# Kernel optimization log

Hardware: AMD Instinct MI355X
Metric: run time of the kernel (lower is better)

## Reference

```python
import jax, jax.numpy as jnp
import numpy as np

NUM_LAYERS = 3
INPUT_SIZE = 64
EMB = 128
NUM_CAT = 128          # must equal EMB for the W_e_proj assignment to shape-check
NUM_QUERIES = 1
INIT_SCALE = 0.02
KERNEL_PARAM = 1.0     # referenced-but-undefined in source; standard alpha=1
B = 16
N = 2048
D = INPUT_SIZE + 2 * EMB                 # 320, transformer embedding dim
F_IN = INPUT_SIZE + NUM_CAT + EMB        # 320, raw input feature dim


def setup_inputs() -> dict:
    key = jax.random.key(0)
    k = jax.random.split(key, 6)
    x = jax.random.normal(k[0], (B, F_IN, N), dtype=jnp.float32)
    embedding_matrix = jax.random.normal(k[1], (EMB, NUM_CAT), dtype=jnp.float32)
    W_Q = jax.random.normal(k[2], (NUM_LAYERS, 1, D, D), dtype=jnp.float32) * INIT_SCALE
    W_K = jax.random.normal(k[3], (NUM_LAYERS, 1, D, D), dtype=jnp.float32) * INIT_SCALE
    W_V = jax.random.normal(k[4], (NUM_LAYERS, 1, D, D), dtype=jnp.float32) * INIT_SCALE
    P = jax.random.normal(k[5], (NUM_LAYERS, 1, D, D), dtype=jnp.float32) * INIT_SCALE
    return {"x": x, "embedding_matrix": embedding_matrix,
            "W_Q": W_Q, "W_K": W_K, "W_V": W_V, "P": P}


def _build_We(embedding_matrix):
    W = jnp.zeros((D, F_IN), dtype=embedding_matrix.dtype)
    W = W.at[:INPUT_SIZE, :INPUT_SIZE].set(jnp.eye(INPUT_SIZE, dtype=W.dtype))
    W = W.at[D - EMB:, F_IN - EMB:].set(jnp.eye(EMB, dtype=W.dtype))
    # rows [input_size : D-emb], cols [input_size : F-num_categories]
    W = W.at[INPUT_SIZE:D - EMB, INPUT_SIZE:F_IN - NUM_CAT].set(embedding_matrix)
    return W


def reference(x, embedding_matrix, W_Q, W_K, W_V, P):
    W = _build_We(embedding_matrix)
    h = jnp.einsum('df,bfn->bdn', W, x)                        # [B, D, N]
    for nl in range(NUM_LAYERS):
        key = h[:, :, :-NUM_QUERIES]                           # include_query=False
        value = key
        query = h
        n_context = key.shape[-1]
        Q = jnp.einsum('id,bdm->bim', W_Q[nl, 0], query)       # [B, D, N]
        K = jnp.einsum('id,bdn->bin', W_K[nl, 0], key)         # [B, D, M]
        V = jnp.einsum('id,bdn->bin', W_V[nl, 0], value)       # [B, D, M]
        # linear kernel scores
        scores = KERNEL_PARAM * jnp.einsum('bim,bin->bmn', Q, K)  # [B, N, M]
        attn = jnp.einsum('bin,bmn->bim', V, scores) / n_context  # [B, D, N]
        h = h + jnp.einsum('ji,bim->bjm', P[nl, 0], attn)
    f = h[:, -EMB:, :]                                         # [B, EMB, N] (squeeze no-op for B>1)
    logits = jnp.einsum('bdn,dc->bnc', f, embedding_matrix)    # [B, N, C]
    predictions = jax.nn.softmax(logits, axis=-1)
    return logits, predictions
```

## Files before the change

kernel.cpp:

```cpp
#include <hip/hip_runtime.h>
#include <math.h>

typedef long long ll;
typedef unsigned int uint;
typedef unsigned short ushort;
typedef __attribute__((ext_vector_type(4))) float f32x4;
typedef __attribute__((ext_vector_type(8))) short bf16x8;

#define SZ 102400LL
#define RS 40960LL

__device__ inline void split2(float v, ushort& h, ushort& l)
{
    uint u = __float_as_uint(v);
    uint uh = u + (0x7FFFu + ((u >> 16) & 1u));
    h = (ushort)(uh >> 16);
    float hf = __uint_as_float((uint)h << 16);
    float d = v - hf;
    uint ud = __float_as_uint(d);
    l = (ushort)((ud + (0x7FFFu + ((ud >> 16) & 1u))) >> 16);
}
__device__ inline float us2f(ushort h, ushort l)
{
    return __uint_as_float((uint)h << 16) + __uint_as_float((uint)l << 16);
}

__global__ __launch_bounds__(256) void gram_sp_k(
    const float* __restrict__ x, float* __restrict__ part,
    const float* __restrict__ Wq, const float* __restrict__ Wk,
    const float* __restrict__ Wv, const float* __restrict__ P,
    const float* __restrict__ emb,
    ushort* __restrict__ WqTs, ushort* __restrict__ WkTs, ushort* __restrict__ WvTs,
    ushort* __restrict__ Ps, ushort* __restrict__ embs, ushort* __restrict__ embTs,
    float* __restrict__ q0, ushort* __restrict__ xTh)
{
    __shared__ __align__(16) char smem[20480];
    int bid0 = blockIdx.x, tid = threadIdx.x;
    if (bid0 < 960) {
        ushort* Ah  = (ushort*)smem;
        ushort* Al_ = Ah + 2560;
        ushort* Bh  = Al_ + 2560;
        ushort* Bl_ = Bh + 2560;
        int flat = bid0;
        int swz = (flat & 7) * 120 + (flat >> 3);
        int b = swz / 60;
        int rr = swz - b * 60;
        int p = rr / 15, t = rr - p * 15;
        int ti = 0, rem = t;
        while (rem >= 5 - ti) { rem -= 5 - ti; ++ti; }
        int tj = ti + rem;
        int i0 = ti * 64, j0 = tj * 64;
        bool diag = (ti == tj);
        const float* X = x + (ll)b * 320 * 2048;
        int wv = tid >> 6, lane = tid & 63;
        int lr = lane & 15, kb = (lane >> 4) * 8;
        int cr = tid >> 2, ck = (tid & 3) * 8;
        f32x4 hh[4], hl[4], lh[4];
        f32x4 zz = {0.f, 0.f, 0.f, 0.f};
        #pragma unroll
        for (int f = 0; f < 4; ++f) { hh[f] = zz; hl[f] = zz; lh[f] = zz; }
        const ushort* BhS = diag ? Ah : Bh;
        const ushort* BlS = diag ? Al_ : Bl_;

        for (int it = 0; it < 16; ++it) {
            int kg0 = p * 512 + it * 32;
            {
                const float* src = X + (ll)(i0 + cr) * 2048 + kg0 + ck;
                float4 v0 = *(const float4*)src;
                float4 v1 = *(const float4*)(src + 4);
                float vals[8] = {v0.x,v0.y,v0.z,v0.w,v1.x,v1.y,v1.z,v1.w};
                if (kg0 + ck + 7 >= 2047) {
                    #pragma unroll
                    for (int u = 0; u < 8; ++u) if (kg0 + ck + u >= 2047) vals[u] = 0.f;
                }
                bf16x8 hv, lv;
                #pragma unroll
                for (int u = 0; u < 8; ++u) { ushort h, l; split2(vals[u], h, l);
                                              hv[u] = (short)h; lv[u] = (short)l; }
                *(bf16x8*)&Ah[cr * 40 + ck] = hv;
                *(bf16x8*)&Al_[cr * 40 + ck] = lv;
            }
            if (!diag) {
                const float* src = X + (ll)(j0 + cr) * 2048 + kg0 + ck;
                float4 v0 = *(const float4*)src;
                float4 v1 = *(const float4*)(src + 4);
                float vals[8] = {v0.x,v0.y,v0.z,v0.w,v1.x,v1.y,v1.z,v1.w};
                if (kg0 + ck + 7 >= 2047) {
                    #pragma unroll
                    for (int u = 0; u < 8; ++u) if (kg0 + ck + u >= 2047) vals[u] = 0.f;
                }
                bf16x8 hv, lv;
                #pragma unroll
                for (int u = 0; u < 8; ++u) { ushort h, l; split2(vals[u], h, l);
                                              hv[u] = (short)h; lv[u] = (short)l; }
                *(bf16x8*)&Bh[cr * 40 + ck] = hv;
                *(bf16x8*)&Bl_[cr * 40 + ck] = lv;
            }
            __syncthreads();
            if (xTh && diag) {
                int nl = tid >> 3, fq = (tid & 7) * 8;
                int n = kg0 + nl;
                bf16x8 v;
                #pragma unroll
                for (int u = 0; u < 8; ++u) v[u] = (short)Ah[(fq + u) * 40 + nl];
                if (n == 2047) {
                    #pragma unroll
                    for (int u = 0; u < 8; ++u) {
                        ushort h, l;
                        split2(X[(ll)(i0 + fq + u) * 2048 + 2047], h, l);
                        v[u] = (short)h;
                    }
                }
                *(bf16x8*)&xTh[((ll)b * 2048 + n) * 320 + i0 + fq] = v;
            }
            bf16x8 ah = *(const bf16x8*)&Ah[(wv * 16 + lr) * 40 + kb];
            bf16x8 al = *(const bf16x8*)&Al_[(wv * 16 + lr) * 40 + kb];
            #pragma unroll
            for (int f = 0; f < 4; ++f) {
                bf16x8 bh_ = *(const bf16x8*)&BhS[(f * 16 + lr) * 40 + kb];
                bf16x8 bl_ = *(const bf16x8*)&BlS[(f * 16 + lr) * 40 + kb];
                hh[f] = __builtin_amdgcn_mfma_f32_16x16x32_bf16(ah, bh_, hh[f], 0, 0, 0);
                hl[f] = __builtin_amdgcn_mfma_f32_16x16x32_bf16(ah, bl_, hl[f], 0, 0, 0);
                lh[f] = __builtin_amdgcn_mfma_f32_16x16x32_bf16(al, bh_, lh[f], 0, 0, 0);
            }
            __syncthreads();
        }
        float* out = part + (((ll)p * 16 + b) * 15 + t) * 4096;
        int orow0 = wv * 16 + (lane >> 4) * 4;
        #pragma unroll
        for (int f = 0; f < 4; ++f) {
            int col = f * 16 + lr;
            #pragma unroll
            for (int r = 0; r < 4; ++r)
                out[(orow0 + r) * 64 + col] = hh[f][r] + hl[f][r] + lh[f][r];
        }
        return;
    }
    int bid = bid0 - 960;
    float (*T)[65] = (float(*)[65])smem;
    if (bid < 225) {
        int m = bid / 25, t = bid % 25;
        const float* mats[3] = {Wq, Wk, Wv};
        ushort* dsts[3] = {WqTs, WkTs, WvTs};
        const float* src = mats[m / 3] + (ll)(m % 3) * SZ;
        ushort* dst = dsts[m / 3] + (ll)(m % 3) * SZ;
        int r0 = (t / 5) * 64, c0 = (t % 5) * 64;
        #pragma unroll
        for (int s = 0; s < 4; ++s) {
            int idx = s * 256 + tid;
            int r = idx >> 4, cq = (idx & 15) * 4;
            *(float4*)&T[r][cq] = *(const float4*)(src + (ll)(r0 + r) * 320 + c0 + cq);
        }
        __syncthreads();
        {
            int c = tid >> 2, kq = (tid & 3) * 16;
            bf16x8 h0, h1, l0, l1;
            #pragma unroll
            for (int u = 0; u < 8; ++u) {
                ushort h, l;
                split2(T[kq + u][c], h, l);     h0[u] = (short)h; l0[u] = (short)l;
                split2(T[kq + 8 + u][c], h, l); h1[u] = (short)h; l1[u] = (short)l;
            }
            ushort* dh = dst + (ll)(c0 + c) * 320 + r0 + kq;
            *(bf16x8*)dh = h0; *(bf16x8*)(dh + 8) = h1;
            *(bf16x8*)(dh + 3 * SZ) = l0; *(bf16x8*)(dh + 3 * SZ + 8) = l1;
        }
    } else if (bid < 375) {
        ll off = (ll)(bid - 225) * 2048 + tid * 8;
        float4 v0 = *(const float4*)(P + off);
        float4 v1 = *(const float4*)(P + off + 4);
        float vals[8] = {v0.x,v0.y,v0.z,v0.w,v1.x,v1.y,v1.z,v1.w};
        bf16x8 hv, lv;
        #pragma unroll
        for (int u = 0; u < 8; ++u) { ushort h,l; split2(vals[u],h,l);
                                      hv[u]=(short)h; lv[u]=(short)l; }
        *(bf16x8*)(Ps + off) = hv;
        *(bf16x8*)(Ps + off + 3 * SZ) = lv;
    } else if (bid < 383) {
        ll off = (ll)(bid - 375) * 2048 + tid * 8;
        float4 v0 = *(const float4*)(emb + off);
        float4 v1 = *(const float4*)(emb + off + 4);
        float vals[8] = {v0.x,v0.y,v0.z,v0.w,v1.x,v1.y,v1.z,v1.w};
        bf16x8 hv, lv;
        #pragma unroll
        for (int u = 0; u < 8; ++u) { ushort h,l; split2(vals[u],h,l);
                                      hv[u]=(short)h; lv[u]=(short)l; }
        *(bf16x8*)(embs + off) = hv;
        *(bf16x8*)(embs + off + 16384) = lv;
    } else if (bid < 387) {
        int t = bid - 383;
        int r0 = (t >> 1) * 64, c0 = (t & 1) * 64;
        {
            int r = tid >> 2, cq = (tid & 3) * 4;
            *(float4*)&T[r][cq]      = *(const float4*)(emb + (ll)(r0 + r) * 128 + c0 + cq);
            *(float4*)&T[r][cq + 16] = *(const float4*)(emb + (ll)(r0 + r) * 128 + c0 + cq + 16);
            *(float4*)&T[r][cq + 32] = *(const float4*)(emb + (ll)(r0 + r) * 128 + c0 + cq + 32);
            *(float4*)&T[r][cq + 48] = *(const float4*)(emb + (ll)(r0 + r) * 128 + c0 + cq + 48);
        }
        __syncthreads();
        {
            int c = tid >> 2, kq = (tid & 3) * 16;
            bf16x8 h0, h1, l0, l1;
            #pragma unroll
            for (int u = 0; u < 8; ++u) {
                ushort h, l;
                split2(T[kq + u][c], h, l);     h0[u]=(short)h; l0[u]=(short)l;
                split2(T[kq + 8 + u][c], h, l); h1[u]=(short)h; l1[u]=(short)l;
            }
            ushort* dh = embTs + (ll)(c0 + c) * 128 + r0 + kq;
            *(bf16x8*)dh = h0; *(bf16x8*)(dh + 8) = h1;
            *(bf16x8*)(dh + 16384) = l0; *(bf16x8*)(dh + 16384 + 8) = l1;
        }
    } else {
        ll base = (ll)(bid - 387) * 2048;
        #pragma unroll
        for (int s = 0; s < 8; ++s) {
            ll id = base + s * 256 + tid;
            int c = (int)(id / 320), i = (int)(id % 320);
            q0[id] = (i >= 192) ? emb[(ll)(i - 192) * 128 + c] : 0.f;
        }
    }
}

__global__ __launch_bounds__(256) void gram_red_k(const float* __restrict__ part,
                                                  ushort* __restrict__ GxS,
                                                  ushort* __restrict__ T1s)
{
    int bt = blockIdx.x;
    int b = bt / 15, t = bt % 15;
    int ti = 0, rem = t;
    while (rem >= 5 - ti) { rem -= 5 - ti; ++ti; }
    int tj = ti + rem;
    int i0 = ti * 64, j0 = tj * 64;
    int tid = threadIdx.x;
    int tx = tid & 15, rg = tid >> 4;
    bool wi = (ti == 0 || ti >= 3);
    bool wj = (tj == 0 || tj >= 3);
    ushort* Gb = GxS + (ll)b * SZ;
    ushort* Tsb = T1s + (ll)b * SZ;
    #pragma unroll
    for (int m = 0; m < 4; ++m) {
        int r = rg * 4 + m;
        float s[4] = {};
        for (int p = 0; p < 4; ++p) {
            const float* src = part + (((ll)p * 16 + b) * 15 + t) * 4096 + r * 64 + tx * 4;
            float4 v = *(const float4*)src;
            s[0]+=v.x; s[1]+=v.y; s[2]+=v.z; s[3]+=v.w;
        }
        #pragma unroll
        for (int u = 0; u < 4; ++u) {
            ushort h, l; split2(s[u], h, l);
            ll rd = (ll)(i0 + r) * 320 + j0 + tx * 4 + u;
            ll rt = (ll)(j0 + tx * 4 + u) * 320 + (i0 + r);
            Gb[rd] = h; Gb[rd + 16 * SZ] = l;
            Gb[rt] = h; Gb[rt + 16 * SZ] = l;
            if (wi) { Tsb[rd] = h; Tsb[rd + 16 * SZ] = l; }
            if (wj) { Tsb[rt] = h; Tsb[rt + 16 * SZ] = l; }
        }
    }
}

struct CJob {
    const ushort *Ah, *Bh;
    const void *Ci, *Ci2;
    float* C; ushort* Cs;
    ll aB, bB, ciB, ci2B, cB, csB;
    ll aLo, bLo, csLo, ciLo, ci2Lo;
    int aS, bS, ciS, ci2S, cS, csS;
    int K, tN, tpb, flags;
    int swzQ, swzR;
    float alpha;
};
struct CPack { CJob j[4]; };

__global__ __launch_bounds__(256) void mchain_k(CPack jp, int c0, int c1, int c2)
{
    int bid = blockIdx.x;
    int ji, local;
    if (bid < c0)      { ji = 0; local = bid; }
    else if (bid < c1) { ji = 1; local = bid - c0; }
    else if (bid < c2) { ji = 2; local = bid - c1; }
    else               { ji = 3; local = bid - c2; }
    CJob j = jp.j[ji];
    int xcd = local & 7, sidx = local >> 3;
    int base = (xcd < j.swzR) ? xcd * (j.swzQ + 1)
                              : j.swzR * (j.swzQ + 1) + (xcd - j.swzR) * j.swzQ;
    int swz = base + sidx;
    int bz = swz / j.tpb;
    int t = swz - bz * j.tpb;
    int i0 = (t / j.tN) * 64, j0 = (t % j.tN) * 64;
    int tid = threadIdx.x;
    int wv = tid >> 6, lane = tid & 63;
    int lr = lane & 15, kb = (lane >> 4) * 8;
    f32x4 hh[4], cx[4];
    f32x4 zz = {0.f,0.f,0.f,0.f};
    #pragma unroll
    for (int f = 0; f < 4; ++f) { hh[f] = zz; cx[f] = zz; }

    __shared__ __align__(16) ushort Bsh[2][2][2560];

    if (j.K > 0) {
        int srow = tid >> 2, skq = (tid & 3) * 8;
        const ushort* Bg = j.Bh + (ll)bz * j.bB + (ll)(j0 + srow) * j.bS + skq;
        const ushort* Ar = j.Ah + (ll)bz * j.aB + (ll)(i0 + wv * 16 + lr) * j.aS + kb;
        bf16x8 svh, svl, ah, al, ahn, aln;
        svh = *(const bf16x8*)Bg;
        svl = *(const bf16x8*)(Bg + j.bLo);
        *(bf16x8*)&Bsh[0][0][srow * 40 + skq] = svh;
        *(bf16x8*)&Bsh[0][1][srow * 40 + skq] = svl;
        ah = *(const bf16x8*)Ar;
        al = *(const bf16x8*)(Ar + j.aLo);
        __syncthreads();
        int nit = j.K >> 5;
        for (int it = 0; it < nit; ++it) {
            int cur = it & 1;
            bool more = (it + 1 < nit);
            if (more) {
                int k1 = (it + 1) << 5;
                svh = *(const bf16x8*)(Bg + k1);
                svl = *(const bf16x8*)(Bg + j.bLo + k1);
                ahn = *(const bf16x8*)(Ar + k1);
                aln = *(const bf16x8*)(Ar + j.aLo + k1);
            }
            #pragma unroll
            for (int f = 0; f < 4; ++f) {
                bf16x8 bh = *(const bf16x8*)&Bsh[cur][0][(f * 16 + lr) * 40 + kb];
                bf16x8 bl = *(const bf16x8*)&Bsh[cur][1][(f * 16 + lr) * 40 + kb];
                hh[f] = __builtin_amdgcn_mfma_f32_16x16x32_bf16(ah, bh, hh[f], 0, 0, 0);
                cx[f] = __builtin_amdgcn_mfma_f32_16x16x32_bf16(ah, bl, cx[f], 0, 0, 0);
                cx[f] = __builtin_amdgcn_mfma_f32_16x16x32_bf16(al, bh, cx[f], 0, 0, 0);
            }
            if (more) {
                *(bf16x8*)&Bsh[cur ^ 1][0][srow * 40 + skq] = svh;
                *(bf16x8*)&Bsh[cur ^ 1][1][srow * 40 + skq] = svl;
                ah = ahn; al = aln;
            }
            __syncthreads();
        }
    }
    const float* Cif = (const float*)j.Ci;
    const ushort* Ciu = (const ushort*)j.Ci;
    const float* Ci2f = (const float*)j.Ci2;
    const ushort* Ci2u = (const ushort*)j.Ci2;
    float* Cp = j.C + (ll)bz * j.cB;
    ushort* Csp = j.Cs + (ll)bz * j.csB;
    int r0 = i0 + wv * 16 + ((lane >> 4) << 2);
    #pragma unroll
    for (int f = 0; f < 4; ++f) {
        int col = j0 + f * 16 + lr;
        #pragma unroll
        for (int r = 0; r < 4; ++r) {
            int row = r0 + r;
            float v = j.alpha * (hh[f][r] + cx[f][r]);
            if (j.flags & 1)
                v += Cif[(ll)bz * j.ciB + (ll)row * j.ciS + col];
            if (j.flags & 32) {
                const ushort* p = Ciu + (ll)bz * j.ciB + (ll)row * j.ciS + col;
                v += us2f(p[0], p[j.ciLo]);
            }
            if (j.flags & 64) {
                const ushort* b2 = Ci2u + (ll)bz * j.ci2B;
                if (j.flags & 2) { const ushort* p = b2 + (ll)row * j.ci2S + col;
                                   v += us2f(p[0], p[j.ci2Lo]); }
                if (j.flags & 4) { const ushort* p = b2 + (ll)col * j.ci2S + row;
                                   v += us2f(p[0], p[j.ci2Lo]); }
            } else {
                if (j.flags & 2) v += Ci2f[(ll)bz * j.ci2B + (ll)row * j.ci2S + col];
                if (j.flags & 4) v += Ci2f[(ll)bz * j.ci2B + (ll)col * j.ci2S + row];
            }
            if (j.flags & 8) Cp[(ll)row * j.cS + col] = v;
            if (j.flags & 16) {
                ushort h, l; split2(v, h, l);
                ushort* p = Csp + (ll)row * j.csS + col;
                p[0] = h; p[j.csLo] = l;
            }
        }
    }
}

__global__ __launch_bounds__(256) void logits_v4_k(const ushort* __restrict__ xTh,
                                                   const ushort* __restrict__ LBs,
                                                   float* __restrict__ logits,
                                                   float* __restrict__ pred)
{
    int flat = blockIdx.x;
    int swzb = (flat & 7) * 128 + (flat >> 3);
    int b = swzb >> 6;
    int i0 = (swzb & 63) * 32;
    const ushort* XT = xTh + (ll)b * 2048 * 320;
    const ushort* LB = LBs + (ll)b * RS;
    __shared__ float SB[32][132];
    __shared__ float pmL[2][32], psL[2][32];
    int tid = threadIdx.x;
    int wv = tid >> 6, lane = tid & 63;
    int lr = lane & 15, g = lane >> 4, kb = g * 8;
    int rowg = (wv & 1) * 16, ch = wv >> 1, colh = ch * 64;
    f32x4 hh[4], cx[4];
    f32x4 zz = {0.f,0.f,0.f,0.f};
    #pragma unroll
    for (int f = 0; f < 4; ++f) { hh[f] = zz; cx[f] = zz; }
    const ushort* Ar = XT + (ll)(i0 + rowg + lr) * 320 + kb;
    for (int it = 0; it < 10; ++it) {
        bf16x8 ah = *(const bf16x8*)(Ar + it * 32);
        const ushort* B0 = LB + (ll)(colh + lr) * 320 + it * 32 + kb;
        bf16x8 b0h = *(const bf16x8*)B0;
        bf16x8 b0l = *(const bf16x8*)(B0 + 16 * RS);
        bf16x8 b1h = *(const bf16x8*)(B0 + 16 * 320);
        bf16x8 b1l = *(const bf16x8*)(B0 + 16 * 320 + 16 * RS);
        bf16x8 b2h = *(const bf16x8*)(B0 + 32 * 320);
        bf16x8 b2l = *(const bf16x8*)(B0 + 32 * 320 + 16 * RS);
        bf16x8 b3h = *(const bf16x8*)(B0 + 48 * 320);
        bf16x8 b3l = *(const bf16x8*)(B0 + 48 * 320 + 16 * RS);
        hh[0] = __builtin_amdgcn_mfma_f32_16x16x32_bf16(ah, b0h, hh[0], 0, 0, 0);
        cx[0] = __builtin_amdgcn_mfma_f32_16x16x32_bf16(ah, b0l, cx[0], 0, 0, 0);
        hh[1] = __builtin_amdgcn_mfma_f32_16x16x32_bf16(ah, b1h, hh[1], 0, 0, 0);
        cx[1] = __builtin_amdgcn_mfma_f32_16x16x32_bf16(ah, b1l, cx[1], 0, 0, 0);
        hh[2] = __builtin_amdgcn_mfma_f32_16x16x32_bf16(ah, b2h, hh[2], 0, 0, 0);
        cx[2] = __builtin_amdgcn_mfma_f32_16x16x32_bf16(ah, b2l, cx[2], 0, 0, 0);
        hh[3] = __builtin_amdgcn_mfma_f32_16x16x32_bf16(ah, b3h, hh[3], 0, 0, 0);
        cx[3] = __builtin_amdgcn_mfma_f32_16x16x32_bf16(ah, b3l, cx[3], 0, 0, 0);
    }
    float v[4][4];
    #pragma unroll
    for (int r = 0; r < 4; ++r)
        #pragma unroll
        for (int f = 0; f < 4; ++f) v[r][f] = hh[f][r] + cx[f][r];
    #pragma unroll
    for (int r = 0; r < 4; ++r) {
        float m = fmaxf(fmaxf(v[r][0], v[r][1]), fmaxf(v[r][2], v[r][3]));
        #pragma unroll
        for (int off = 8; off; off >>= 1) m = fmaxf(m, __shfl_xor(m, off));
        if (lr == 0) pmL[ch][rowg + g * 4 + r] = m;
    }
    __syncthreads();
    float ev[4][4], inv[4];
    #pragma unroll
    for (int r = 0; r < 4; ++r) {
        int blr = rowg + g * 4 + r;
        float mx = fmaxf(pmL[0][blr], pmL[1][blr]);
        float s = 0.f;
        #pragma unroll
        for (int f = 0; f < 4; ++f) { ev[r][f] = expf(v[r][f] - mx); s += ev[r][f]; }
        #pragma unroll
        for (int off = 8; off; off >>= 1) s += __shfl_xor(s, off);
        if (lr == 0) psL[ch][blr] = s;
    }
    __syncthreads();
    #pragma unroll
    for (int r = 0; r < 4; ++r) {
        int blr = rowg + g * 4 + r;
        inv[r] = 1.f / (psL[0][blr] + psL[1][blr]);
    }
    #pragma unroll
    for (int r = 0; r < 4; ++r)
        #pragma unroll
        for (int f = 0; f < 4; ++f)
            SB[rowg + g * 4 + r][colh + f * 16 + lr] = v[r][f];
    __syncthreads();
    #pragma unroll
    for (int s = 0; s < 4; ++s) {
        int idx = s * 256 + tid;
        int row = idx >> 5, cq = (idx & 31) * 4;
        *(float4*)(logits + ((ll)b * 2048 + i0 + row) * 128 + cq) = *(float4*)&SB[row][cq];
    }
    __syncthreads();
    #pragma unroll
    for (int r = 0; r < 4; ++r)
        #pragma unroll
        for (int f = 0; f < 4; ++f)
            SB[rowg + g * 4 + r][colh + f * 16 + lr] = ev[r][f] * inv[r];
    __syncthreads();
    #pragma unroll
    for (int s = 0; s < 4; ++s) {
        int idx = s * 256 + tid;
        int row = idx >> 5, cq = (idx & 31) * 4;
        *(float4*)(pred + ((ll)b * 2048 + i0 + row) * 128 + cq) = *(float4*)&SB[row][cq];
    }
}

__global__ __launch_bounds__(256) void logits_mfma_k(const float* __restrict__ x,
                                                     const ushort* __restrict__ LBs,
                                                     float* __restrict__ logits,
                                                     float* __restrict__ pred)
{
    int flat = blockIdx.x;
    int swzb = (flat & 7) * 128 + (flat >> 3);
    int b = swzb >> 6;
    int i0 = (swzb & 63) * 32;
    const float* X = x + (ll)b * 320 * 2048;
    const ushort* LB = LBs + (ll)b * RS;
    __shared__ float Xs_[2][32][33];
    __shared__ float SB[32][132];
    __shared__ float pmL[2][32], psL[2][32];
    int tid = threadIdx.x;
    int wv = tid >> 6, lane = tid & 63;
    int lr = lane & 15, g = lane >> 4, kb = g * 8;
    int rowg = (wv & 1) * 16, ch = wv >> 1, colh = ch * 64;
    int lkk = tid >> 3, lq = (tid & 7) * 4;
    f32x4 hh[4], cx[4];
    f32x4 zz = {0.f,0.f,0.f,0.f};
    #pragma unroll
    for (int f = 0; f < 4; ++f) { hh[f] = zz; cx[f] = zz; }
    float4 pa;
    auto glb = [&](int k0) {
        pa = *(const float4*)(X + (ll)(k0 + lkk) * 2048 + i0 + lq);
    };
    auto stl = [&](int buf) {
        float* p = &Xs_[buf][lkk][lq];
        p[0] = pa.x; p[1] = pa.y; p[2] = pa.z; p[3] = pa.w;
    };
    glb(0); stl(0);
    __syncthreads();
    for (int it = 0; it < 10; ++it) {
        int cur = it & 1;
        if (it < 9) glb((it + 1) * 32);
        const ushort* B0 = LB + (ll)(colh + lr) * 320 + it * 32 + kb;
        bf16x8 b0h = *(const bf16x8*)B0;
        bf16x8 b0l = *(const bf16x8*)(B0 + 16 * RS);
        bf16x8 b1h = *(const bf16x8*)(B0 + 16 * 320);
        bf16x8 b1l = *(const bf16x8*)(B0 + 16 * 320 + 16 * RS);
        bf16x8 b2h = *(const bf16x8*)(B0 + 32 * 320);
        bf16x8 b2l = *(const bf16x8*)(B0 + 32 * 320 + 16 * RS);
        bf16x8 b3h = *(const bf16x8*)(B0 + 48 * 320);
        bf16x8 b3l = *(const bf16x8*)(B0 + 48 * 320 + 16 * RS);
        bf16x8 ah, al;
        #pragma unroll
        for (int u = 0; u < 8; ++u) {
            ushort h, l;
            split2(Xs_[cur][kb + u][rowg + lr], h, l);
            ah[u] = (short)h; al[u] = (short)l;
        }
        hh[0] = __builtin_amdgcn_mfma_f32_16x16x32_bf16(ah, b0h, hh[0], 0, 0, 0);
        cx[0] = __builtin_amdgcn_mfma_f32_16x16x32_bf16(ah, b0l, cx[0], 0, 0, 0);
        cx[0] = __builtin_amdgcn_mfma_f32_16x16x32_bf16(al, b0h, cx[0], 0, 0, 0);
        hh[1] = __builtin_amdgcn_mfma_f32_16x16x32_bf16(ah, b1h, hh[1], 0, 0, 0);
        cx[1] = __builtin_amdgcn_mfma_f32_16x16x32_bf16(ah, b1l, cx[1], 0, 0, 0);
        cx[1] = __builtin_amdgcn_mfma_f32_16x16x32_bf16(al, b1h, cx[1], 0, 0, 0);
        hh[2] = __builtin_amdgcn_mfma_f32_16x16x32_bf16(ah, b2h, hh[2], 0, 0, 0);
        cx[2] = __builtin_amdgcn_mfma_f32_16x16x32_bf16(ah, b2l, cx[2], 0, 0, 0);
        cx[2] = __builtin_amdgcn_mfma_f32_16x16x32_bf16(al, b2h, cx[2], 0, 0, 0);
        hh[3] = __builtin_amdgcn_mfma_f32_16x16x32_bf16(ah, b3h, hh[3], 0, 0, 0);
        cx[3] = __builtin_amdgcn_mfma_f32_16x16x32_bf16(ah, b3l, cx[3], 0, 0, 0);
        cx[3] = __builtin_amdgcn_mfma_f32_16x16x32_bf16(al, b3h, cx[3], 0, 0, 0);
        if (it < 9) stl(cur ^ 1);
        __syncthreads();
    }
    float v[4][4];
    #pragma unroll
    for (int r = 0; r < 4; ++r)
        #pragma unroll
        for (int f = 0; f < 4; ++f) v[r][f] = hh[f][r] + cx[f][r];
    #pragma unroll
    for (int r = 0; r < 4; ++r) {
        float m = fmaxf(fmaxf(v[r][0], v[r][1]), fmaxf(v[r][2], v[r][3]));
        #pragma unroll
        for (int off = 8; off; off >>= 1) m = fmaxf(m, __shfl_xor(m, off));
        if (lr == 0) pmL[ch][rowg + g * 4 + r] = m;
    }
    __syncthreads();
    float ev[4][4], inv[4];
    #pragma unroll
    for (int r = 0; r < 4; ++r) {
        int blr = rowg + g * 4 + r;
        float mx = fmaxf(pmL[0][blr], pmL[1][blr]);
        float s = 0.f;
        #pragma unroll
        for (int f = 0; f < 4; ++f) { ev[r][f] = expf(v[r][f] - mx); s += ev[r][f]; }
        #pragma unroll
        for (int off = 8; off; off >>= 1) s += __shfl_xor(s, off);
        if (lr == 0) psL[ch][blr] = s;
    }
    __syncthreads();
    #pragma unroll
    for (int r = 0; r < 4; ++r) {
        int blr = rowg + g * 4 + r;
        inv[r] = 1.f / (psL[0][blr] + psL[1][blr]);
    }
    #pragma unroll
    for (int r = 0; r < 4; ++r)
        #pragma unroll
        for (int f = 0; f < 4; ++f)
            SB[rowg + g * 4 + r][colh + f * 16 + lr] = v[r][f];
    __syncthreads();
    #pragma unroll
    for (int s = 0; s < 4; ++s) {
        int idx = s * 256 + tid;
        int row = idx >> 5, cq = (idx & 31) * 4;
        *(float4*)(logits + ((ll)b * 2048 + i0 + row) * 128 + cq) = *(float4*)&SB[row][cq];
    }
    __syncthreads();
    #pragma unroll
    for (int r = 0; r < 4; ++r)
        #pragma unroll
        for (int f = 0; f < 4; ++f)
            SB[rowg + g * 4 + r][colh + f * 16 + lr] = ev[r][f] * inv[r];
    __syncthreads();
    #pragma unroll
    for (int s = 0; s < 4; ++s) {
        int idx = s * 256 + tid;
        int row = idx >> 5, cq = (idx & 31) * 4;
        *(float4*)(pred + ((ll)b * 2048 + i0 + row) * 128 + cq) = *(float4*)&SB[row][cq];
    }
}

extern "C" void kernel_launch(void* const* d_in, const int* in_sizes, int n_in,
                              void* d_out, int out_size, void* d_ws, size_t ws_size,
                              hipStream_t stream)
{
    const float* x   = (const float*)d_in[0];
    const float* emb = (const float*)d_in[1];
    const float* Wq  = (const float*)d_in[2];
    const float* Wk  = (const float*)d_in[3];
    const float* Wv  = (const float*)d_in[4];
    const float* P   = (const float*)d_in[5];

    float* logits = (float*)d_out;
    float* pred   = logits + (ll)16 * 2048 * 128;

    float* w = (float*)d_ws;
    auto takef = [&](ll n) { float* p = w; w += n; return p; };
    ushort* GxS  = (ushort*)takef(16 * SZ);
    ushort* T1s  = (ushort*)takef(16 * SZ);
    ushort* Gs   = (ushort*)takef(16 * SZ);
    ushort* As   = (ushort*)takef(16 * SZ);
    ushort* Us   = (ushort*)takef(16 * SZ);
    float*  ATsF = takef(48 * SZ);
    ushort* ATs  = (ushort*)ATsF;
    ushort* PVs  = (ushort*)takef(3 * SZ);
    ushort* KQTs = (ushort*)takef(3 * SZ);
    ushort* KQs  = (ushort*)takef(3 * SZ);
    ushort* Ps   = (ushort*)takef(3 * SZ);
    ushort* WqTs = (ushort*)takef(3 * SZ);
    ushort* WkTs = (ushort*)takef(3 * SZ);
    ushort* WvTs = (ushort*)takef(3 * SZ);
    ushort* embs = (ushort*)takef(16384);
    ushort* embTs= (ushort*)takef(16384);
    float*  q0f  = takef(RS);
    ushort* q1s  = (ushort*)takef(16 * RS);
    ushort* q2s  = (ushort*)takef(16 * RS);
    ushort* LBs  = (ushort*)takef(16 * RS);
    ll base_floats = (ll)(w - (float*)d_ws);
    ushort* xTh = nullptr;
    if (ws_size >= (size_t)(base_floats + 5242880) * 4)
        xTh = (ushort*)takef(5242880);
    ushort* Xs   = GxS;
    ushort* Zts  = T1s;
    float*  part = ATsF;
    ushort* q3s  = q1s;
    const float cinv = 1.f / 2047.f;

    auto JB = [](const ushort* Ah, ll aB, int aS, ll aLo,
                 const ushort* Bh, ll bB, int bS, ll bLo,
                 int K, int tM, int tN, float alpha, int flags,
                 const void* Ci, ll ciB, int ciS, ll ciLo,
                 const void* Ci2, ll ci2B, int ci2S, ll ci2Lo,
                 float* C, ll cB, int cS,
                 ushort* Cs, ll csB, int csS, ll csLo) {
        CJob j;
        j.Ah = Ah; j.Bh = Bh;
        j.Ci = Ci; j.Ci2 = Ci2; j.C = C; j.Cs = Cs;
        j.aB = aB; j.bB = bB; j.ciB = ciB; j.ci2B = ci2B; j.cB = cB; j.csB = csB;
        j.aLo = aLo; j.bLo = bLo; j.csLo = csLo; j.ciLo = ciLo; j.ci2Lo = ci2Lo;
        j.aS = aS; j.bS = bS; j.ciS = ciS; j.ci2S = ci2S; j.cS = cS; j.csS = csS;
        j.K = K; j.tN = tN; j.tpb = tM * tN; j.flags = flags; j.alpha = alpha;
        j.swzQ = 0; j.swzR = 0;
        return j;
    };
    auto fire = [&](const CJob* js, const int* nb, int n) {
        CPack jp;
        int cum[4], tot = 0;
        for (int i = 0; i < 4; ++i) {
            jp.j[i] = js[i < n ? i : 0];
            if (i < n) { jp.j[i].swzQ = nb[i] >> 3; jp.j[i].swzR = nb[i] & 7; }
            tot += (i < n ? nb[i] : 0);
            cum[i] = tot;
        }
        mchain_k<<<tot, 256, 0, stream>>>(jp, cum[0], cum[1], cum[2]);
    };

    gram_sp_k<<<1367, 256, 0, stream>>>(x, part, Wq, Wk, Wv, P, emb,
                                        WqTs, WkTs, WvTs, Ps, embs, embTs, q0f, xTh);
    gram_red_k<<<240, 256, 0, stream>>>(part, GxS, T1s);
    {
        CJob js[4] = {
            JB(embs, 0, 128, 16384,  GxS + 64, SZ, 320, 16*SZ,  128, 2, 5, 1.f, 16,
               0,0,0,0, 0,0,0,0,  0,0,0,  T1s + 64*320, SZ, 320, 16*SZ),
            JB(Ps, SZ, 320, 3*SZ,  WvTs, SZ, 320, 3*SZ,  320, 5, 5, 1.f, 16,
               0,0,0,0, 0,0,0,0,  0,0,0,  PVs, SZ, 320, 3*SZ),
            JB(WqTs, SZ, 320, 3*SZ,  WkTs, SZ, 320, 3*SZ,  320, 5, 5, 1.f, 16,
               0,0,0,0, 0,0,0,0,  0,0,0,  KQTs, SZ, 320, 3*SZ),
            JB(WkTs, SZ, 320, 3*SZ,  WqTs, SZ, 320, 3*SZ,  320, 5, 5, 1.f, 16,
               0,0,0,0, 0,0,0,0,  0,0,0,  KQs, SZ, 320, 3*SZ)};
        int nb[4] = {160, 75, 75, 75};
        fire(js, nb, 4);
    }
    {
        CJob js[3] = {
            JB(T1s + 64, SZ, 320, 16*SZ,  embs, 0, 128, 16384,  128, 5, 2, 1.f, 16,
               0,0,0,0, 0,0,0,0,  0,0,0,  Gs + 64, SZ, 320, 16*SZ),
            JB(0,0,0,0, 0,0,0,0,  0, 5, 1, 0.f, 32|16,
               T1s, SZ, 320, 16*SZ, 0,0,0,0,  0,0,0,  Gs, SZ, 320, 16*SZ),
            JB(0,0,0,0, 0,0,0,0,  0, 5, 2, 0.f, 32|16,
               T1s + 192, SZ, 320, 16*SZ, 0,0,0,0,  0,0,0,  Gs + 192, SZ, 320, 16*SZ)};
        int nb[3] = {160, 80, 160};
        fire(js, nb, 3);
    }
    for (int l = 0; l < 3; ++l) {
        const ushort* PVl = PVs + (ll)l * SZ;
        const ushort* KQTl = KQTs + (ll)l * SZ;
        const ushort* KQl = KQs + (ll)l * SZ;
        ushort* ATl = ATs + (ll)l * 16 * SZ;
        if (l < 2) {
            CJob s1[2] = {
                JB(PVl, 0, 320, 3*SZ,  Gs, SZ, 320, 16*SZ,  320, 5, 5, 1.f, 16,
                   0,0,0,0, 0,0,0,0,  0,0,0,  Xs, SZ, 320, 16*SZ),
                JB(Gs, SZ, 320, 16*SZ,  KQl, 0, 320, 3*SZ,  320, 5, 5, 1.f, 16,
                   0,0,0,0, 0,0,0,0,  0,0,0,  Zts, SZ, 320, 16*SZ)};
            int n1[2] = {400, 400};
            fire(s1, n1, 2);
            CJob s2[3] = {
                JB(Xs, SZ, 320, 16*SZ,  KQTl, 0, 320, 3*SZ,  320, 5, 5, cinv, 16,
                   0,0,0,0, 0,0,0,0,  0,0,0,  As, SZ, 320, 16*SZ),
                JB(KQTl, 0, 320, 3*SZ,  Xs, SZ, 320, 16*SZ,  320, 5, 5, cinv, 16,
                   0,0,0,0, 0,0,0,0,  0,0,0,  ATl, SZ, 320, 48*SZ),
                JB(Xs, SZ, 320, 16*SZ,  Zts, SZ, 320, 16*SZ,  320, 5, 5, cinv, 16,
                   0,0,0,0, 0,0,0,0,  0,0,0,  Us, SZ, 320, 16*SZ)};
            int n2[3] = {400, 400, 400};
            fire(s2, n2, 3);
            CJob s3[1] = {
                JB(Us, SZ, 320, 16*SZ,  As, SZ, 320, 16*SZ,  320, 5, 5, 1.f, 16|32|2|4|64,
                   Gs, SZ, 320, 16*SZ,  Us, SZ, 320, 16*SZ,  0,0,0,  Gs, SZ, 320, 16*SZ)};
            int n3[1] = {400};
            fire(s3, n3, 1);
        } else {
            CJob s1[1] = {
                JB(PVl, 0, 320, 3*SZ,  Gs, SZ, 320, 16*SZ,  320, 5, 5, 1.f, 16,
                   0,0,0,0, 0,0,0,0,  0,0,0,  Xs, SZ, 320, 16*SZ)};
            int n1[1] = {400};
            fire(s1, n1, 1);
            CJob s2[1] = {
                JB(KQTl, 0, 320, 3*SZ,  Xs, SZ, 320, 16*SZ,  320, 5, 5, cinv, 16,
                   0,0,0,0, 0,0,0,0,  0,0,0,  ATl, SZ, 320, 48*SZ)};
            int n2[1] = {400};
            fire(s2, n2, 1);
        }
    }
    {
        CJob js[1] = {
            JB(embTs, 0, 128, 16384,  ATs + 2*16*SZ + 192, SZ, 320, 48*SZ,  128, 2, 5, 1.f, 1|16,
               q0f, 0, 320, 0, 0,0,0,0,  0,0,0,  q1s, RS, 320, 16*RS)};
        int nb[1] = {160};
        fire(js, nb, 1);
    }
    {
        CJob js[1] = {
            JB(q1s, RS, 320, 16*RS,  ATs + 1*16*SZ, SZ, 320, 48*SZ,  320, 2, 5, 1.f, 32|16,
               q1s, RS, 320, 16*RS, 0,0,0,0,  0,0,0,  q2s, RS, 320, 16*RS)};
        int nb[1] = {160};
        fire(js, nb, 1);
    }
    {
        CJob js[1] = {
            JB(q2s, RS, 320, 16*RS,  ATs, SZ, 320, 48*SZ,  320, 2, 5, 1.f, 32|16,
               q2s, RS, 320, 16*RS, 0,0,0,0,  0,0,0,  q3s, RS, 320, 16*RS)};
        int nb[1] = {160};
        fire(js, nb, 1);
    }
    {
        CJob js[3] = {
            JB(q3s + 64, RS, 320, 16*RS,  embTs, 0, 128, 16384,  128, 2, 2, 1.f, 16,
               0,0,0,0, 0,0,0,0,  0,0,0,  LBs + 64, RS, 320, 16*RS),
            JB(0,0,0,0, 0,0,0,0,  0, 2, 1, 0.f, 32|16,
               q3s, RS, 320, 16*RS, 0,0,0,0,  0,0,0,  LBs, RS, 320, 16*RS),
            JB(0,0,0,0, 0,0,0,0,  0, 2, 2, 0.f, 32|16,
               q3s + 192, RS, 320, 16*RS, 0,0,0,0,  0,0,0,  LBs + 192, RS, 320, 16*RS)};
        int nb[3] = {64, 32, 64};
        fire(js, nb, 3);
    }
    if (xTh)
        logits_v4_k<<<1024, 256, 0, stream>>>(xTh, LBs, logits, pred);
    else
        logits_mfma_k<<<1024, 256, 0, stream>>>(x, LBs, logits, pred);
}
```

Baseline: 320.8 us.

## Fold two per-layer attention matrices into one product and double-buffer logits loads

In the final layer, a new job multiplies the per-layer attention matrices (ATs times As, plus an added term) into a combined M01 matrix, launched alongside an existing job. This lets the query-row chain apply one 320x320 multiply instead of two sequential dependent launches. The logits kernel also gains software double-buffered register prefetching of its bf16 operands so global loads overlap the MFMAs. The cost is an extra 400-block batched 320x320 GEMM over all batches and higher register pressure in the logits kernel.

```diff
diff --git a/kernel.cpp b/kernel.cpp
--- a/kernel.cpp
+++ b/kernel.cpp
@@ -378,7 +378,7 @@
     }
 }
 
-__global__ __launch_bounds__(256) void logits_v4_k(const ushort* __restrict__ xTh,
+__global__ __launch_bounds__(256) void logits_v5_k(const ushort* __restrict__ xTh,
                                                    const ushort* __restrict__ LBs,
                                                    float* __restrict__ logits,
                                                    float* __restrict__ pred)
@@ -400,25 +400,37 @@
     #pragma unroll
     for (int f = 0; f < 4; ++f) { hh[f] = zz; cx[f] = zz; }
     const ushort* Ar = XT + (ll)(i0 + rowg + lr) * 320 + kb;
-    for (int it = 0; it < 10; ++it) {
-        bf16x8 ah = *(const bf16x8*)(Ar + it * 32);
-        const ushort* B0 = LB + (ll)(colh + lr) * 320 + it * 32 + kb;
-        bf16x8 b0h = *(const bf16x8*)B0;
-        bf16x8 b0l = *(const bf16x8*)(B0 + 16 * RS);
-        bf16x8 b1h = *(const bf16x8*)(B0 + 16 * 320);
-        bf16x8 b1l = *(const bf16x8*)(B0 + 16 * 320 + 16 * RS);
-        bf16x8 b2h = *(const bf16x8*)(B0 + 32 * 320);
-        bf16x8 b2l = *(const bf16x8*)(B0 + 32 * 320 + 16 * RS);
-        bf16x8 b3h = *(const bf16x8*)(B0 + 48 * 320);
-        bf16x8 b3l = *(const bf16x8*)(B0 + 48 * 320 + 16 * RS);
-        hh[0] = __builtin_amdgcn_mfma_f32_16x16x32_bf16(ah, b0h, hh[0], 0, 0, 0);
-        cx[0] = __builtin_amdgcn_mfma_f32_16x16x32_bf16(ah, b0l, cx[0], 0, 0, 0);
-        hh[1] = __builtin_amdgcn_mfma_f32_16x16x32_bf16(ah, b1h, hh[1], 0, 0, 0);
-        cx[1] = __builtin_amdgcn_mfma_f32_16x16x32_bf16(ah, b1l, cx[1], 0, 0, 0);
-        hh[2] = __builtin_amdgcn_mfma_f32_16x16x32_bf16(ah, b2h, hh[2], 0, 0, 0);
-        cx[2] = __builtin_amdgcn_mfma_f32_16x16x32_bf16(ah, b2l, cx[2], 0, 0, 0);
-        hh[3] = __builtin_amdgcn_mfma_f32_16x16x32_bf16(ah, b3h, hh[3], 0, 0, 0);
-        cx[3] = __builtin_amdgcn_mfma_f32_16x16x32_bf16(ah, b3l, cx[3], 0, 0, 0);
+    const ushort* Bp = LB + (ll)(colh + lr) * 320 + kb;
+
+    bf16x8 aC, c0h, c0l, c1h, c1l, c2h, c2l, c3h, c3l;
+    bf16x8 aN, n0h, n0l, n1h, n1l, n2h, n2l, n3h, n3l;
+    auto LD = [&](int it, bf16x8& A_, bf16x8& B0h, bf16x8& B0l, bf16x8& B1h, bf16x8& B1l,
+                  bf16x8& B2h, bf16x8& B2l, bf16x8& B3h, bf16x8& B3l) {
+        A_ = *(const bf16x8*)(Ar + it * 32);
+        const ushort* q = Bp + it * 32;
+        B0h = *(const bf16x8*)q;              B0l = *(const bf16x8*)(q + 16 * RS);
+        B1h = *(const bf16x8*)(q + 16*320);   B1l = *(const bf16x8*)(q + 16*320 + 16*RS);
+        B2h = *(const bf16x8*)(q + 32*320);   B2l = *(const bf16x8*)(q + 32*320 + 16*RS);
+        B3h = *(const bf16x8*)(q + 48*320);   B3l = *(const bf16x8*)(q + 48*320 + 16*RS);
+    };
+    auto MM = [&](bf16x8& A_, bf16x8& B0h, bf16x8& B0l, bf16x8& B1h, bf16x8& B1l,
+                  bf16x8& B2h, bf16x8& B2l, bf16x8& B3h, bf16x8& B3l) {
+        hh[0] = __builtin_amdgcn_mfma_f32_16x16x32_bf16(A_, B0h, hh[0], 0, 0, 0);
+        cx[0] = __builtin_amdgcn_mfma_f32_16x16x32_bf16(A_, B0l, cx[0], 0, 0, 0);
+        hh[1] = __builtin_amdgcn_mfma_f32_16x16x32_bf16(A_, B1h, hh[1], 0, 0, 0);
+        cx[1] = __builtin_amdgcn_mfma_f32_16x16x32_bf16(A_, B1l, cx[1], 0, 0, 0);
+        hh[2] = __builtin_amdgcn_mfma_f32_16x16x32_bf16(A_, B2h, hh[2], 0, 0, 0);
+        cx[2] = __builtin_amdgcn_mfma_f32_16x16x32_bf16(A_, B2l, cx[2], 0, 0, 0);
+        hh[3] = __builtin_amdgcn_mfma_f32_16x16x32_bf16(A_, B3h, hh[3], 0, 0, 0);
+        cx[3] = __builtin_amdgcn_mfma_f32_16x16x32_bf16(A_, B3l, cx[3], 0, 0, 0);
+    };
+    LD(0, aC, c0h, c0l, c1h, c1l, c2h, c2l, c3h, c3l);
+    #pragma unroll
+    for (int it = 0; it < 10; it += 2) {
+        if (it + 1 < 10) LD(it + 1, aN, n0h, n0l, n1h, n1l, n2h, n2l, n3h, n3l);
+        MM(aC, c0h, c0l, c1h, c1l, c2h, c2l, c3h, c3l);
+        if (it + 2 < 10) LD(it + 2, aC, c0h, c0l, c1h, c1l, c2h, c2l, c3h, c3l);
+        if (it + 1 < 10) MM(aN, n0h, n0l, n1h, n1l, n2h, n2l, n3h, n3l);
     }
     float v[4][4];
     #pragma unroll
@@ -646,7 +658,7 @@
     ushort* Xs   = GxS;
     ushort* Zts  = T1s;
     float*  part = ATsF;
-    ushort* q3s  = q1s;
+    ushort* M01s = Us;
     const float cinv = 1.f / 2047.f;
 
     auto JB = [](const ushort* Ah, ll aB, int aS, ll aLo,
@@ -733,11 +745,14 @@
             int n3[1] = {400};
             fire(s3, n3, 1);
         } else {
-            CJob s1[1] = {
+            CJob s1[2] = {
                 JB(PVl, 0, 320, 3*SZ,  Gs, SZ, 320, 16*SZ,  320, 5, 5, 1.f, 16,
-                   0,0,0,0, 0,0,0,0,  0,0,0,  Xs, SZ, 320, 16*SZ)};
-            int n1[1] = {400};
-            fire(s1, n1, 1);
+                   0,0,0,0, 0,0,0,0,  0,0,0,  Xs, SZ, 320, 16*SZ),
+                JB(ATs, SZ, 320, 48*SZ,  As, SZ, 320, 16*SZ,  320, 5, 5, 1.f, 16|32|2|64,
+                   ATs + 16*SZ, SZ, 320, 48*SZ,  ATs, SZ, 320, 48*SZ,
+                   0,0,0,  M01s, SZ, 320, 16*SZ)};
+            int n1[2] = {400, 400};
+            fire(s1, n1, 2);
             CJob s2[1] = {
                 JB(KQTl, 0, 320, 3*SZ,  Xs, SZ, 320, 16*SZ,  320, 5, 5, cinv, 16,
                    0,0,0,0, 0,0,0,0,  0,0,0,  ATl, SZ, 320, 48*SZ)};
@@ -754,31 +769,24 @@
     }
     {
         CJob js[1] = {
-            JB(q1s, RS, 320, 16*RS,  ATs + 1*16*SZ, SZ, 320, 48*SZ,  320, 2, 5, 1.f, 32|16,
+            JB(q1s, RS, 320, 16*RS,  M01s, SZ, 320, 16*SZ,  320, 2, 5, 1.f, 32|16,
                q1s, RS, 320, 16*RS, 0,0,0,0,  0,0,0,  q2s, RS, 320, 16*RS)};
         int nb[1] = {160};
         fire(js, nb, 1);
     }
     {
-        CJob js[1] = {
-            JB(q2s, RS, 320, 16*RS,  ATs, SZ, 320, 48*SZ,  320, 2, 5, 1.f, 32|16,
-               q2s, RS, 320, 16*RS, 0,0,0,0,  0,0,0,  q3s, RS, 320, 16*RS)};
-        int nb[1] = {160};
-        fire(js, nb, 1);
-    }
-    {
         CJob js[3] = {
-            JB(q3s + 64, RS, 320, 16*RS,  embTs, 0, 128, 16384,  128, 2, 2, 1.f, 16,
+            JB(q2s + 64, RS, 320, 16*RS,  embTs, 0, 128, 16384,  128, 2, 2, 1.f, 16,
                0,0,0,0, 0,0,0,0,  0,0,0,  LBs + 64, RS, 320, 16*RS),
             JB(0,0,0,0, 0,0,0,0,  0, 2, 1, 0.f, 32|16,
-               q3s, RS, 320, 16*RS, 0,0,0,0,  0,0,0,  LBs, RS, 320, 16*RS),
+               q2s, RS, 320, 16*RS, 0,0,0,0,  0,0,0,  LBs, RS, 320, 16*RS),
             JB(0,0,0,0, 0,0,0,0,  0, 2, 2, 0.f, 32|16,
-               q3s + 192, RS, 320, 16*RS, 0,0,0,0,  0,0,0,  LBs + 192, RS, 320, 16*RS)};
+               q2s + 192, RS, 320, 16*RS, 0,0,0,0,  0,0,0,  LBs + 192, RS, 320, 16*RS)};
         int nb[3] = {64, 32, 64};
         fire(js, nb, 3);
     }
     if (xTh)
-        logits_v4_k<<<1024, 256, 0, stream>>>(xTh, LBs, logits, pred);
+        logits_v5_k<<<1024, 256, 0, stream>>>(xTh, LBs, logits, pred);
     else
         logits_mfma_k<<<1024, 256, 0, stream>>>(x, LBs, logits, pred);
 }
```

After: 319.6 us. Within noise of the previous version (-0.4%).
